# Performance work log

Measured on AMD Instinct MI355X. Metric: run time of the kernel, lower is better.

## Reference

```python
import jax, jax.numpy as jnp
import numpy as np

B, H_IN, H_OUT, SEQ_LEN = 256, 512, 512, 512


def setup_inputs() -> dict:
    key = jax.random.key(0)
    k1, k2, k3, k4, k5 = jax.random.split(key, 5)
    s = 1.0 / np.sqrt(H_OUT)  # torch GRU init scale
    return {
        "x": jax.random.normal(k1, (B, H_IN), dtype=jnp.float32),
        "W_ih": jax.random.uniform(k2, (3 * H_OUT, H_IN), jnp.float32, -s, s),
        "W_hh": jax.random.uniform(k3, (3 * H_OUT, H_OUT), jnp.float32, -s, s),
        "b_ih": jax.random.uniform(k4, (3 * H_OUT,), jnp.float32, -s, s),
        "b_hh": jax.random.uniform(k5, (3 * H_OUT,), jnp.float32, -s, s),
        "seq_len": SEQ_LEN,
    }


def reference(x, W_ih, W_hh, b_ih, b_hh, seq_len):
    # bridge: ReLU, then the same vector is fed at every timestep, so the
    # input-to-hidden projection is computed ONCE and reused across the scan.
    xr = jax.nn.relu(x)                       # [B, H_in]
    gi = xr @ W_ih.T + b_ih                   # [B, 3*H_out], constant over time
    Hh = W_hh.shape[1]
    gi_r, gi_z, gi_n = gi[:, :Hh], gi[:, Hh:2 * Hh], gi[:, 2 * Hh:]

    h0 = jnp.zeros((x.shape[0], Hh), dtype=x.dtype)

    def step(h, _):
        gh = h @ W_hh.T + b_hh                # [B, 3*H_out]
        gh_r, gh_z, gh_n = gh[:, :Hh], gh[:, Hh:2 * Hh], gh[:, 2 * Hh:]
        r = jax.nn.sigmoid(gi_r + gh_r)
        z = jax.nn.sigmoid(gi_z + gh_z)
        n = jnp.tanh(gi_n + r * gh_n)
        h_new = (1.0 - z) * n + z * h
        return h_new, h_new

    _, hs = jax.lax.scan(step, h0, None, length=seq_len)  # [S, B, H_out]
    return jnp.transpose(hs, (1, 0, 2))                   # [B, S, H_out]
```

## Files before the change

kernel.cpp:

```cpp
#include <hip/hip_runtime.h>


typedef __attribute__((ext_vector_type(8))) short short8;
typedef __attribute__((ext_vector_type(4))) float f32x4;
typedef __attribute__((ext_vector_type(4))) unsigned int u32x4;
typedef unsigned short ushort_t;
typedef unsigned int uint_t;
typedef unsigned long long u64_t;

#define NG 16
#define NM 16
#define NB 16
#define NJ 32
#define TPB 384
#define SPIN_MAX (1u << 16)
#define ABORT_IDX 8192
#define GBUF_BASE 16384
#define GRP_U32 4096
#define BUF_U32 65536

#define ALD(P) __hip_atomic_load((P), __ATOMIC_RELAXED, __HIP_MEMORY_SCOPE_AGENT)
#define AST(P, V) __hip_atomic_store((P), (V), __ATOMIC_RELAXED, __HIP_MEMORY_SCOPE_AGENT)

__device__ __forceinline__ ushort_t bf16_rne(float f) {
  uint_t u = __float_as_uint(f);
  return (ushort_t)((u + 0x7fffu + ((u >> 16) & 1u)) >> 16);
}
__device__ __forceinline__ float bf16f(ushort_t h) {
  return __uint_as_float(((uint_t)h) << 16);
}
__device__ __forceinline__ int gRow(int rs, int m) {
  int base = m * NJ;
  if (rs < 32) return base + rs;
  if (rs < 64) return 512 + base + (rs - 32);
  return 1024 + base + (rs - 64);
}

template <bool LO>
__device__ __forceinline__ void loadW(short8* dst, const float* __restrict__ W,
                                      int tile, int m, int lane) {
  int rs = tile * 16 + (lane & 15);
  const float* p = W + (size_t)gRow(rs, m) * 512 + ((lane >> 4) << 3);
#pragma unroll
  for (int c = 0; c < 16; ++c) {
    const float* pc = p + c * 32;
    short8 o;
#pragma unroll
    for (int i = 0; i < 8; ++i) {
      float v = pc[i];
      ushort_t hi = bf16_rne(v);
      o[i] = LO ? (short)bf16_rne(v - bf16f(hi)) : (short)hi;
    }
    dst[c] = o;
  }
}

__global__ __launch_bounds__(TPB, 1) void gru_kernel(
    const float* __restrict__ x, const float* __restrict__ Wih,
    const float* __restrict__ Whh, const float* __restrict__ bih,
    const float* __restrict__ bhh, float* __restrict__ out,
    uint_t* __restrict__ wsp, int NT) {
  __shared__ __align__(16) uint_t s_pb[4096];
  __shared__ __align__(16) uint_t s_xlo[4096];
  __shared__ float s_gi[96 * 17];
  __shared__ float s_gh[96 * 17];
  __shared__ float s_hloc[NB * NJ];
  __shared__ float s_bhh[NJ];
  __shared__ int s_stop;

  const int tid = threadIdx.x;
  const int lane = tid & 63;
  const int w = tid >> 6;
  const int bid = blockIdx.x;
  const int g = bid & 15;
  const int m = bid >> 4;
  const int me = (g << 4) + m;
  if (NT <= 0) return;

  uint_t* flags = wsp;
  uint_t* gbuf = wsp + GBUF_BASE;

  for (int i = tid; i < 1024; i += TPB) {
    int b = i >> 6, k0 = (i & 63) << 3;
    const float* px = x + (size_t)(g * NB + b) * 512 + k0;
    u32x4 vh, vl;
#pragma unroll
    for (int jj = 0; jj < 4; ++jj) {
      float f0 = px[2 * jj], f1 = px[2 * jj + 1];
      f0 = f0 > 0.f ? f0 : 0.f;
      f1 = f1 > 0.f ? f1 : 0.f;
      ushort_t h0 = bf16_rne(f0), h1 = bf16_rne(f1);
      vh[jj] = (uint_t)h0 | ((uint_t)h1 << 16);
      vl[jj] = (uint_t)bf16_rne(f0 - bf16f(h0)) |
               ((uint_t)bf16_rne(f1 - bf16f(h1)) << 16);
    }
    int c = k0 >> 5, kk = k0 & 31;
    int base = c * 1024 + ((((b << 6) + (kk << 1))) ^ ((b & 7) << 4));
    *(u32x4*)((char*)s_pb + base) = vh;
    *(u32x4*)((char*)s_xlo + base) = vl;
  }
  if (tid < NJ) s_bhh[tid] = bhh[1024 + m * NJ + tid];
  if (tid == 0) s_stop = 0;
  __syncthreads();

  short8 wA[16], wB[16];
  const f32x4 vzero = {0.f, 0.f, 0.f, 0.f};
  const int bcol = lane & 15;
  const int roff = ((bcol << 6) + ((lane >> 4) << 4)) ^ ((bcol & 7) << 4);
  const char* pb = (const char*)s_pb;
  const char* pxl = (const char*)s_xlo;

  f32x4 acc0 = vzero, acc1 = vzero;
  if (w < 3) {
    loadW<false>(wA, Wih, 2 * w, m, lane);
    loadW<false>(wB, Wih, 2 * w + 1, m, lane);
    {
      f32x4 a0h = vzero, a0l = vzero, a1h = vzero, a1l = vzero;
#pragma unroll
      for (int c = 0; c < 16; ++c) {
        short8 bh = *(const short8*)(pb + c * 1024 + roff);
        short8 bl = *(const short8*)(pxl + c * 1024 + roff);
        a0h = __builtin_amdgcn_mfma_f32_16x16x32_bf16(wA[c], bh, a0h, 0, 0, 0);
        a1h = __builtin_amdgcn_mfma_f32_16x16x32_bf16(wB[c], bh, a1h, 0, 0, 0);
        a0l = __builtin_amdgcn_mfma_f32_16x16x32_bf16(wA[c], bl, a0l, 0, 0, 0);
        a1l = __builtin_amdgcn_mfma_f32_16x16x32_bf16(wB[c], bl, a1l, 0, 0, 0);
      }
      acc0 = a0h + a0l;
      acc1 = a1h + a1l;
    }
    loadW<true>(wA, Wih, 2 * w, m, lane);
    loadW<true>(wB, Wih, 2 * w + 1, m, lane);
#pragma unroll
    for (int c = 0; c < 16; ++c) {
      short8 bh = *(const short8*)(pb + c * 1024 + roff);
      acc0 = __builtin_amdgcn_mfma_f32_16x16x32_bf16(wA[c], bh, acc0, 0, 0, 0);
      acc1 = __builtin_amdgcn_mfma_f32_16x16x32_bf16(wB[c], bh, acc1, 0, 0, 0);
    }
  }
  __syncthreads();
  if (w < 3) {
    int drow = (lane >> 4) << 2;
#pragma unroll
    for (int q = 0; q < 4; ++q) {
      int rs0 = 2 * w * 16 + drow + q, rs1 = rs0 + 16;
      int g0 = gRow(rs0, m), g1 = gRow(rs1, m);
      s_gi[rs0 * 17 + bcol] = acc0[q] + bih[g0] + (rs0 < 64 ? bhh[g0] : 0.f);
      s_gi[rs1 * 17 + bcol] = acc1[q] + bih[g1] + (rs1 < 64 ? bhh[g1] : 0.f);
    }
    loadW<false>(wA, Whh, 2 * w, m, lane);
    loadW<false>(wB, Whh, 2 * w + 1, m, lane);
  }
  for (int i = tid; i < 4096; i += TPB) s_pb[i] = 0u;
  for (int i = tid; i < NB * NJ; i += TPB) s_hloc[i] = 0.f;
  __syncthreads();

  const size_t outRow = (size_t)NT * 512;
  float* outBase = out + (size_t)(g * NB) * outRow + m * NJ;

  for (int t = 0; t < NT; ++t) {
    if (w < 3) {
      f32x4 aE0 = vzero, aO0 = vzero, aE1 = vzero, aO1 = vzero;
#pragma unroll
      for (int p = 0; p < 16; p += 2) {
        short8 b0 = *(const short8*)(pb + p * 1024 + roff);
        short8 b1 = *(const short8*)(pb + (p + 1) * 1024 + roff);
        aE0 = __builtin_amdgcn_mfma_f32_16x16x32_bf16(wA[p], b0, aE0, 0, 0, 0);
        aE1 = __builtin_amdgcn_mfma_f32_16x16x32_bf16(wB[p], b0, aE1, 0, 0, 0);
        aO0 = __builtin_amdgcn_mfma_f32_16x16x32_bf16(wA[p + 1], b1, aO0, 0, 0, 0);
        aO1 = __builtin_amdgcn_mfma_f32_16x16x32_bf16(wB[p + 1], b1, aO1, 0, 0, 0);
      }
      f32x4 r0 = aE0 + aO0, r1 = aE1 + aO1;
      int drow = (lane >> 4) << 2;
#pragma unroll
      for (int q = 0; q < 4; ++q) {
        s_gh[(2 * w * 16 + drow + q) * 17 + bcol] = r0[q];
        s_gh[((2 * w + 1) * 16 + drow + q) * 17 + bcol] = r1[q];
      }
    }
    __syncthreads();

    const int et = tid - 256;
    float hn[4];
    int eb_ = 0, ej0 = 0;
    if (et >= 0) {
      int b = et >> 3, j0 = (et & 7) << 2;
      eb_ = b;
      ej0 = j0;
#pragma unroll
      for (int e = 0; e < 4; ++e) {
        int j = j0 + e;
        float pr = s_gi[j * 17 + b] + s_gh[j * 17 + b];
        float pz = s_gi[(32 + j) * 17 + b] + s_gh[(32 + j) * 17 + b];
        float r = 1.f / (1.f + __expf(-pr));
        float z = 1.f / (1.f + __expf(-pz));
        float pn =
            s_gi[(64 + j) * 17 + b] + r * (s_gh[(64 + j) * 17 + b] + s_bhh[j]);
        float n = 1.f - 2.f / (1.f + __expf(2.f * pn));
        hn[e] = n + z * (s_hloc[b * 32 + j] - n);
        s_hloc[b * 32 + j] = hn[e];
      }
      uint_t w0 = (uint_t)bf16_rne(hn[0]) | ((uint_t)bf16_rne(hn[1]) << 16);
      uint_t w1 = (uint_t)bf16_rne(hn[2]) | ((uint_t)bf16_rne(hn[3]) << 16);
      u64_t pq = (u64_t)w0 | ((u64_t)w1 << 32);
      u64_t* eb64 =
          (u64_t*)(gbuf + (size_t)((t & 1) ^ 1) * BUF_U32 + g * GRP_U32);
      __hip_atomic_store(eb64 + (m << 7) + (eb_ << 3) + (et & 7), pq,
                         __ATOMIC_RELAXED, __HIP_MEMORY_SCOPE_AGENT);
    }
    __syncthreads();

    if (tid == 256)
      AST(&flags[me << 5], (uint_t)(t + 1));
    if (et >= 0) {
      f32x4 ov = {hn[0], hn[1], hn[2], hn[3]};
      __builtin_nontemporal_store(
          ov,
          (f32x4*)(outBase + (size_t)eb_ * outRow + (size_t)t * 512 + ej0));
    }
    if (w < 4 && t + 1 < NT) {
      const uint_t tgt = (uint_t)(t + 1);
      int ok = 1;
      {
        uint_t sp = 0;
        uint_t* fp = flags + (((g << 4) + (w << 2) + (lane & 3)) << 5);
        for (;;) {
          uint_t v = tgt;
          if (lane < 4) v = ALD(fp);
          if (__all((int)(v >= tgt))) break;
          ++sp;
          uint_t ab = 0;
          if ((sp & 127u) == 0u) {
            ab = ALD(&flags[ABORT_IDX]);
            if (sp > SPIN_MAX) {
              AST(&flags[ABORT_IDX], 1u);
              ab = 1;
            }
          }
          if (__any((int)(ab != 0))) {
            if (lane == 0) s_stop = 1;
            ok = 0;
            break;
          }
          __builtin_amdgcn_s_sleep(1);
        }
      }
      if (ok) {
        const u64_t* srcq =
            (const u64_t*)(gbuf + (size_t)((t + 1) & 1) * BUF_U32 +
                           g * GRP_U32) +
            (w << 9);
#define LDI(k)                                                                 \
  __hip_atomic_load(srcq + lane + ((k) << 6), __ATOMIC_RELAXED,                \
                    __HIP_MEMORY_SCOPE_AGENT)
        u64_t q0 = LDI(0), q1 = LDI(1), q2 = LDI(2), q3 = LDI(3);
        u64_t q4 = LDI(4), q5 = LDI(5), q6 = LDI(6), q7 = LDI(7);
#undef LDI
#define STI(k, qq)                                                             \
  {                                                                            \
    uint_t qb = (uint_t)(((w << 9) + lane + ((k) << 6)) << 3);                 \
    *(u64_t*)((char*)s_pb + (qb ^ (((qb >> 6) & 7u) << 4))) = (qq);            \
  }
        STI(0, q0) STI(1, q1) STI(2, q2) STI(3, q3)
        STI(4, q4) STI(5, q5) STI(6, q6) STI(7, q7)
#undef STI
      }
    }
    __syncthreads();
    if (s_stop) break;
  }
}

extern "C" void kernel_launch(void* const* d_in, const int* in_sizes, int n_in,
                              void* d_out, int out_size, void* d_ws,
                              size_t ws_size, hipStream_t stream) {
  const float* x = (const float*)d_in[0];
  const float* Wih = (const float*)d_in[1];
  const float* Whh = (const float*)d_in[2];
  const float* bih = (const float*)d_in[3];
  const float* bhh = (const float*)d_in[4];
  float* out = (float*)d_out;
  int NT = out_size / (256 * 512);
  uint_t* wsp = (uint_t*)d_ws;
  (void)hipMemsetAsync(d_ws, 0, 65536, stream);
  hipLaunchKernelGGL(gru_kernel, dim3(NG * NM), dim3(TPB), 0, stream, x, Wih,
                     Whh, bih, bhh, out, wsp, NT);
}
```

Before: 1.162 ms.

## Replace post-store barrier and step flag with per-wave checksummed flags

Each epilogue wave now publishes its hidden-state slice together with an XOR checksum in a per-wave, parity-indexed 64-bit flag, right after its data store. This removes the block-wide barrier that sat between the data stores and the flag store. Consumers wait for both wave flags, then reload the data until its checksum matches, which handles the case where the flag becomes visible before the data. This shortens the critical path of each recurrent step. In exchange it adds shuffle reductions, possible reload retries, and a checksum-based correctness argument that could in principle miss a collision.

Result: slower. 1.630 ms (+40.3%).

```diff
diff --git a/kernel.cpp b/kernel.cpp
--- a/kernel.cpp
+++ b/kernel.cpp
@@ -13,7 +13,8 @@
 #define NB 16
 #define NJ 32
 #define TPB 384
-#define SPIN_MAX (1u << 16)
+#define POLL_MAX (1u << 14)
+#define VERIFY_MAX 4096u
 #define ABORT_IDX 8192
 #define GBUF_BASE 16384
 #define GRP_U32 4096
@@ -22,6 +23,9 @@
 #define ALD(P) __hip_atomic_load((P), __ATOMIC_RELAXED, __HIP_MEMORY_SCOPE_AGENT)
 #define AST(P, V) __hip_atomic_store((P), (V), __ATOMIC_RELAXED, __HIP_MEMORY_SCOPE_AGENT)
 
+__device__ __forceinline__ uint_t fold64(u64_t q) {
+  return (uint_t)q ^ (uint_t)(q >> 32);
+}
 __device__ __forceinline__ ushort_t bf16_rne(float f) {
   uint_t u = __float_as_uint(f);
   return (ushort_t)((u + 0x7fffu + ((u >> 16) & 1u)) >> 16);
@@ -77,7 +81,8 @@
   const int me = (g << 4) + m;
   if (NT <= 0) return;
 
-  uint_t* flags = wsp;
+  uint_t* flagsu = wsp;
+  u64_t* flq = (u64_t*)wsp;
   uint_t* gbuf = wsp + GBUF_BASE;
 
   for (int i = tid; i < 1024; i += TPB) {
@@ -158,6 +163,7 @@
   float* outBase = out + (size_t)(g * NB) * outRow + m * NJ;
 
   for (int t = 0; t < NT; ++t) {
+    const int par = (t + 1) & 1;
     if (w < 3) {
       f32x4 aE0 = vzero, aO0 = vzero, aE1 = vzero, aO1 = vzero;
 #pragma unroll
@@ -180,12 +186,9 @@
     __syncthreads();
 
     const int et = tid - 256;
-    float hn[4];
-    int eb_ = 0, ej0 = 0;
     if (et >= 0) {
       int b = et >> 3, j0 = (et & 7) << 2;
-      eb_ = b;
-      ej0 = j0;
+      float hn[4];
 #pragma unroll
       for (int e = 0; e < 4; ++e) {
         int j = j0 + e;
@@ -202,67 +205,106 @@
       uint_t w0 = (uint_t)bf16_rne(hn[0]) | ((uint_t)bf16_rne(hn[1]) << 16);
       uint_t w1 = (uint_t)bf16_rne(hn[2]) | ((uint_t)bf16_rne(hn[3]) << 16);
       u64_t pq = (u64_t)w0 | ((u64_t)w1 << 32);
-      u64_t* eb64 =
-          (u64_t*)(gbuf + (size_t)((t & 1) ^ 1) * BUF_U32 + g * GRP_U32);
-      __hip_atomic_store(eb64 + (m << 7) + (eb_ << 3) + (et & 7), pq,
-                         __ATOMIC_RELAXED, __HIP_MEMORY_SCOPE_AGENT);
-    }
-    __syncthreads();
-
-    if (tid == 256)
-      AST(&flags[me << 5], (uint_t)(t + 1));
-    if (et >= 0) {
+      u64_t* eb64 = (u64_t*)(gbuf + (size_t)par * BUF_U32 + g * GRP_U32);
+      AST(eb64 + (m << 7) + (b << 3) + (et & 7), pq);
+      uint_t c32 = fold64(pq);
+#pragma unroll
+      for (int off = 1; off < 64; off <<= 1) c32 ^= __shfl_xor(c32, off);
+      if (lane == 0) {
+        u64_t f = (u64_t)(uint_t)(t + 1) | ((u64_t)c32 << 32);
+        AST(flq + ((size_t)me << 4) + (par << 1) + (w - 4), f);
+      }
       f32x4 ov = {hn[0], hn[1], hn[2], hn[3]};
       __builtin_nontemporal_store(
-          ov,
-          (f32x4*)(outBase + (size_t)eb_ * outRow + (size_t)t * 512 + ej0));
-    }
+          ov, (f32x4*)(outBase + (size_t)b * outRow + (size_t)t * 512 + j0));
+    }
+
     if (w < 4 && t + 1 < NT) {
       const uint_t tgt = (uint_t)(t + 1);
-      int ok = 1;
+      int aborted = 0;
+      uint_t cs = 0;
       {
+        const u64_t* fq =
+            flq + ((size_t)((g << 4) + (w << 2) + (lane & 3)) << 4) +
+            (par << 1);
         uint_t sp = 0;
-        uint_t* fp = flags + (((g << 4) + (w << 2) + (lane & 3)) << 5);
         for (;;) {
-          uint_t v = tgt;
-          if (lane < 4) v = ALD(fp);
-          if (__all((int)(v >= tgt))) break;
+          int rdy = 1;
+          u64_t f0 = 0, f1 = 0;
+          if (lane < 4) {
+            f0 = ALD(fq);
+            f1 = ALD(fq + 1);
+            rdy = ((uint_t)f0 == tgt) && ((uint_t)f1 == tgt);
+          }
+          if (__all(rdy)) {
+            cs = (uint_t)(f0 >> 32) ^ (uint_t)(f1 >> 32);
+            break;
+          }
           ++sp;
           uint_t ab = 0;
-          if ((sp & 127u) == 0u) {
-            ab = ALD(&flags[ABORT_IDX]);
-            if (sp > SPIN_MAX) {
-              AST(&flags[ABORT_IDX], 1u);
+          if ((sp & 7u) == 0u) {
+            ab = ALD(&flagsu[ABORT_IDX]);
+            if (sp > POLL_MAX) {
+              AST(&flagsu[ABORT_IDX], 1u);
               ab = 1;
             }
           }
           if (__any((int)(ab != 0))) {
             if (lane == 0) s_stop = 1;
-            ok = 0;
+            aborted = 1;
             break;
           }
           __builtin_amdgcn_s_sleep(1);
         }
       }
-      if (ok) {
+      if (!aborted) {
         const u64_t* srcq =
-            (const u64_t*)(gbuf + (size_t)((t + 1) & 1) * BUF_U32 +
-                           g * GRP_U32) +
+            (const u64_t*)(gbuf + (size_t)par * BUF_U32 + g * GRP_U32) +
             (w << 9);
-#define LDI(k)                                                                 \
-  __hip_atomic_load(srcq + lane + ((k) << 6), __ATOMIC_RELAXED,                \
-                    __HIP_MEMORY_SCOPE_AGENT)
-        u64_t q0 = LDI(0), q1 = LDI(1), q2 = LDI(2), q3 = LDI(3);
-        u64_t q4 = LDI(4), q5 = LDI(5), q6 = LDI(6), q7 = LDI(7);
-#undef LDI
+        uint_t att = 0;
+        int good = 0;
+        u64_t q0, q1, q2, q3, q4, q5, q6, q7;
+        for (;;) {
+          q0 = ALD(srcq + lane + 0 * 64);
+          q1 = ALD(srcq + lane + 1 * 64);
+          q2 = ALD(srcq + lane + 2 * 64);
+          q3 = ALD(srcq + lane + 3 * 64);
+          q4 = ALD(srcq + lane + 4 * 64);
+          q5 = ALD(srcq + lane + 5 * 64);
+          q6 = ALD(srcq + lane + 6 * 64);
+          q7 = ALD(srcq + lane + 7 * 64);
+          uint_t c0 = fold64(q0 ^ q1), c1 = fold64(q2 ^ q3);
+          uint_t c2 = fold64(q4 ^ q5), c3 = fold64(q6 ^ q7);
+#pragma unroll
+          for (int off = 1; off < 64; off <<= 1) {
+            c0 ^= __shfl_xor(c0, off);
+            c1 ^= __shfl_xor(c1, off);
+            c2 ^= __shfl_xor(c2, off);
+            c3 ^= __shfl_xor(c3, off);
+          }
+          uint_t mysum =
+              (lane & 2) ? ((lane & 1) ? c3 : c2) : ((lane & 1) ? c1 : c0);
+          int ok = (lane < 4) ? (mysum == cs) : 1;
+          if (__all(ok)) {
+            good = 1;
+            break;
+          }
+          if (++att > VERIFY_MAX) {
+            AST(&flagsu[ABORT_IDX], 1u);
+            if (lane == 0) s_stop = 1;
+            break;
+          }
+        }
+        if (good) {
 #define STI(k, qq)                                                             \
   {                                                                            \
     uint_t qb = (uint_t)(((w << 9) + lane + ((k) << 6)) << 3);                 \
     *(u64_t*)((char*)s_pb + (qb ^ (((qb >> 6) & 7u) << 4))) = (qq);            \
   }
-        STI(0, q0) STI(1, q1) STI(2, q2) STI(3, q3)
-        STI(4, q4) STI(5, q5) STI(6, q6) STI(7, q7)
+          STI(0, q0) STI(1, q1) STI(2, q2) STI(3, q3)
+          STI(4, q4) STI(5, q5) STI(6, q6) STI(7, q7)
 #undef STI
+        }
       }
     }
     __syncthreads();
```

## Replace flag-based inter-block handoff with step-tagged data words polled directly

Applied to the files above, without the earlier changes.

Each hidden-state store now packs 32 bits of bf16 data with a 32-bit timestep tag in a single 64-bit atomic word. Consumers poll the data itself until every tag matches, replacing the separate per-block flag store, the extra __syncthreads before it, and the flag spin followed by a second load. This removes one barrier and one global round trip from each recurrent step. In exchange it doubles the bytes exchanged through the global buffer, makes each poll load 16 words per lane, and adds a fixed sleep before polling starts.

Result: slower. 2.609 ms (+124.5%).

```diff
diff --git a/kernel.cpp b/kernel.cpp
--- a/kernel.cpp
+++ b/kernel.cpp
@@ -13,11 +13,11 @@
 #define NB 16
 #define NJ 32
 #define TPB 384
-#define SPIN_MAX (1u << 16)
+#define SWEEP_MAX 8192u
 #define ABORT_IDX 8192
 #define GBUF_BASE 16384
-#define GRP_U32 4096
-#define BUF_U32 65536
+#define PAR_U64 65536
+#define GRP_U64 4096
 
 #define ALD(P) __hip_atomic_load((P), __ATOMIC_RELAXED, __HIP_MEMORY_SCOPE_AGENT)
 #define AST(P, V) __hip_atomic_store((P), (V), __ATOMIC_RELAXED, __HIP_MEMORY_SCOPE_AGENT)
@@ -74,11 +74,10 @@
   const int bid = blockIdx.x;
   const int g = bid & 15;
   const int m = bid >> 4;
-  const int me = (g << 4) + m;
   if (NT <= 0) return;
 
-  uint_t* flags = wsp;
-  uint_t* gbuf = wsp + GBUF_BASE;
+  uint_t* flagsu = wsp;
+  u64_t* gq = (u64_t*)(wsp + GBUF_BASE);
 
   for (int i = tid; i < 1024; i += TPB) {
     int b = i >> 6, k0 = (i & 63) << 3;
@@ -158,6 +157,7 @@
   float* outBase = out + (size_t)(g * NB) * outRow + m * NJ;
 
   for (int t = 0; t < NT; ++t) {
+    const int par = (t + 1) & 1;
     if (w < 3) {
       f32x4 aE0 = vzero, aO0 = vzero, aE1 = vzero, aO1 = vzero;
 #pragma unroll
@@ -180,12 +180,9 @@
     __syncthreads();
 
     const int et = tid - 256;
-    float hn[4];
-    int eb_ = 0, ej0 = 0;
     if (et >= 0) {
       int b = et >> 3, j0 = (et & 7) << 2;
-      eb_ = b;
-      ej0 = j0;
+      float hn[4];
 #pragma unroll
       for (int e = 0; e < 4; ++e) {
         int j = j0 + e;
@@ -199,70 +196,74 @@
         hn[e] = n + z * (s_hloc[b * 32 + j] - n);
         s_hloc[b * 32 + j] = hn[e];
       }
-      uint_t w0 = (uint_t)bf16_rne(hn[0]) | ((uint_t)bf16_rne(hn[1]) << 16);
-      uint_t w1 = (uint_t)bf16_rne(hn[2]) | ((uint_t)bf16_rne(hn[3]) << 16);
-      u64_t pq = (u64_t)w0 | ((u64_t)w1 << 32);
-      u64_t* eb64 =
-          (u64_t*)(gbuf + (size_t)((t & 1) ^ 1) * BUF_U32 + g * GRP_U32);
-      __hip_atomic_store(eb64 + (m << 7) + (eb_ << 3) + (et & 7), pq,
-                         __ATOMIC_RELAXED, __HIP_MEMORY_SCOPE_AGENT);
-    }
-    __syncthreads();
-
-    if (tid == 256)
-      AST(&flags[me << 5], (uint_t)(t + 1));
-    if (et >= 0) {
+      const u64_t tag = (u64_t)(uint_t)(t + 1) << 32;
+      uint_t d0 = (uint_t)bf16_rne(hn[0]) | ((uint_t)bf16_rne(hn[1]) << 16);
+      uint_t d1 = (uint_t)bf16_rne(hn[2]) | ((uint_t)bf16_rne(hn[3]) << 16);
+      u64_t* dst = gq + (size_t)par * PAR_U64 + g * GRP_U64 + m * 256 +
+                   b * 16 + ((et & 7) << 1);
+      AST(dst, (u64_t)d0 | tag);
+      AST(dst + 1, (u64_t)d1 | tag);
       f32x4 ov = {hn[0], hn[1], hn[2], hn[3]};
       __builtin_nontemporal_store(
-          ov,
-          (f32x4*)(outBase + (size_t)eb_ * outRow + (size_t)t * 512 + ej0));
-    }
+          ov, (f32x4*)(outBase + (size_t)b * outRow + (size_t)t * 512 + j0));
+    }
+
     if (w < 4 && t + 1 < NT) {
       const uint_t tgt = (uint_t)(t + 1);
-      int ok = 1;
-      {
-        uint_t sp = 0;
-        uint_t* fp = flags + (((g << 4) + (w << 2) + (lane & 3)) << 5);
-        for (;;) {
-          uint_t v = tgt;
-          if (lane < 4) v = ALD(fp);
-          if (__all((int)(v >= tgt))) break;
-          ++sp;
-          uint_t ab = 0;
-          if ((sp & 127u) == 0u) {
-            ab = ALD(&flags[ABORT_IDX]);
-            if (sp > SPIN_MAX) {
-              AST(&flags[ABORT_IDX], 1u);
-              ab = 1;
-            }
+      const int p = (w << 2) + (lane >> 4);
+      const int kp = lane & 15;
+      const u64_t* src =
+          gq + (size_t)par * PAR_U64 + g * GRP_U64 + p * 256 + kp;
+      u64_t q0, q1, q2, q3, q4, q5, q6, q7, q8, q9, qA, qB, qC, qD, qE, qF;
+      int good = 0;
+      uint_t sweeps = 0;
+      __builtin_amdgcn_s_sleep(6);
+      for (;;) {
+        q0 = ALD(src + 0 * 16);  q1 = ALD(src + 1 * 16);
+        q2 = ALD(src + 2 * 16);  q3 = ALD(src + 3 * 16);
+        q4 = ALD(src + 4 * 16);  q5 = ALD(src + 5 * 16);
+        q6 = ALD(src + 6 * 16);  q7 = ALD(src + 7 * 16);
+        q8 = ALD(src + 8 * 16);  q9 = ALD(src + 9 * 16);
+        qA = ALD(src + 10 * 16); qB = ALD(src + 11 * 16);
+        qC = ALD(src + 12 * 16); qD = ALD(src + 13 * 16);
+        qE = ALD(src + 14 * 16); qF = ALD(src + 15 * 16);
+        uint_t ok =
+            ((uint_t)(q0 >> 32) == tgt) & ((uint_t)(q1 >> 32) == tgt) &
+            ((uint_t)(q2 >> 32) == tgt) & ((uint_t)(q3 >> 32) == tgt) &
+            ((uint_t)(q4 >> 32) == tgt) & ((uint_t)(q5 >> 32) == tgt) &
+            ((uint_t)(q6 >> 32) == tgt) & ((uint_t)(q7 >> 32) == tgt) &
+            ((uint_t)(q8 >> 32) == tgt) & ((uint_t)(q9 >> 32) == tgt) &
+            ((uint_t)(qA >> 32) == tgt) & ((uint_t)(qB >> 32) == tgt) &
+            ((uint_t)(qC >> 32) == tgt) & ((uint_t)(qD >> 32) == tgt) &
+            ((uint_t)(qE >> 32) == tgt) & ((uint_t)(qF >> 32) == tgt);
+        if (__all((int)ok)) {
+          good = 1;
+          break;
+        }
+        ++sweeps;
+        uint_t ab = 0;
+        if ((sweeps & 7u) == 0u) {
+          ab = ALD(&flagsu[ABORT_IDX]);
+          if (sweeps > SWEEP_MAX) {
+            AST(&flagsu[ABORT_IDX], 1u);
+            ab = 1;
           }
-          if (__any((int)(ab != 0))) {
-            if (lane == 0) s_stop = 1;
-            ok = 0;
-            break;
-          }
-          __builtin_amdgcn_s_sleep(1);
         }
-      }
-      if (ok) {
-        const u64_t* srcq =
-            (const u64_t*)(gbuf + (size_t)((t + 1) & 1) * BUF_U32 +
-                           g * GRP_U32) +
-            (w << 9);
-#define LDI(k)                                                                 \
-  __hip_atomic_load(srcq + lane + ((k) << 6), __ATOMIC_RELAXED,                \
-                    __HIP_MEMORY_SCOPE_AGENT)
-        u64_t q0 = LDI(0), q1 = LDI(1), q2 = LDI(2), q3 = LDI(3);
-        u64_t q4 = LDI(4), q5 = LDI(5), q6 = LDI(6), q7 = LDI(7);
-#undef LDI
-#define STI(k, qq)                                                             \
-  {                                                                            \
-    uint_t qb = (uint_t)(((w << 9) + lane + ((k) << 6)) << 3);                 \
-    *(u64_t*)((char*)s_pb + (qb ^ (((qb >> 6) & 7u) << 4))) = (qq);            \
-  }
-        STI(0, q0) STI(1, q1) STI(2, q2) STI(3, q3)
-        STI(4, q4) STI(5, q5) STI(6, q6) STI(7, q7)
-#undef STI
+        if (__any((int)(ab != 0))) {
+          if (lane == 0) s_stop = 1;
+          break;
+        }
+        __builtin_amdgcn_s_sleep(2);
+      }
+      if (good) {
+#define STW(b, qq)                                                             \
+  *(uint_t*)((char*)s_pb + p * 1024 +                                          \
+             ((((b) << 6) + (kp << 2)) ^ (((b)&7) << 4))) = (uint_t)(qq);
+        STW(0, q0)  STW(1, q1)  STW(2, q2)  STW(3, q3)
+        STW(4, q4)  STW(5, q5)  STW(6, q6)  STW(7, q7)
+        STW(8, q8)  STW(9, q9)  STW(10, qA) STW(11, qB)
+        STW(12, qC) STW(13, qD) STW(14, qE) STW(15, qF)
+#undef STW
       }
     }
     __syncthreads();
```

## Restructure GRU step loop to one barrier with MFMA operands read from global

Applied to the files above, without the earlier changes.

The per-step loop is reordered so the elementwise gate update runs first, on a double-buffered s_gh, and the MMA waves then spin on flags and compute the next step's hidden projection. Each MMA lane loads its bf16 hidden-state operands straight from the global exchange buffer into registers, which removes the LDS staging copy and two of the three __syncthreads per step. Producer waves publish per-wave flags after an explicit vmcnt wait, instead of one flag per block after a barrier. The cost is more global atomic loads per lane, more flag polling, a larger register footprint, and a shorter spin/abort limit.

Result: slower. 2.022 ms (+74.1%).

```diff
diff --git a/kernel.cpp b/kernel.cpp
--- a/kernel.cpp
+++ b/kernel.cpp
@@ -13,14 +13,19 @@
 #define NB 16
 #define NJ 32
 #define TPB 384
-#define SPIN_MAX (1u << 16)
+#define SPIN_MAX (1u << 15)
 #define ABORT_IDX 8192
 #define GBUF_BASE 16384
-#define GRP_U32 4096
-#define BUF_U32 65536
+#define PAR_U64 32768
+#define GRP_U64 2048
 
 #define ALD(P) __hip_atomic_load((P), __ATOMIC_RELAXED, __HIP_MEMORY_SCOPE_AGENT)
 #define AST(P, V) __hip_atomic_store((P), (V), __ATOMIC_RELAXED, __HIP_MEMORY_SCOPE_AGENT)
+#define VMWAIT()                                                               \
+  do {                                                                         \
+    asm volatile("s_waitcnt vmcnt(0)" ::: "memory");                           \
+    __builtin_amdgcn_sched_barrier(0);                                         \
+  } while (0)
 
 __device__ __forceinline__ ushort_t bf16_rne(float f) {
   uint_t u = __float_as_uint(f);
@@ -28,6 +33,15 @@
 }
 __device__ __forceinline__ float bf16f(ushort_t h) {
   return __uint_as_float(((uint_t)h) << 16);
+}
+__device__ __forceinline__ short8 mk8(u64_t a, u64_t b) {
+  union {
+    u64_t q[2];
+    short8 s;
+  } u;
+  u.q[0] = a;
+  u.q[1] = b;
+  return u.s;
 }
 __device__ __forceinline__ int gRow(int rs, int m) {
   int base = m * NJ;
@@ -63,7 +77,7 @@
   __shared__ __align__(16) uint_t s_pb[4096];
   __shared__ __align__(16) uint_t s_xlo[4096];
   __shared__ float s_gi[96 * 17];
-  __shared__ float s_gh[96 * 17];
+  __shared__ float s_gh[2][96 * 17];
   __shared__ float s_hloc[NB * NJ];
   __shared__ float s_bhh[NJ];
   __shared__ int s_stop;
@@ -77,8 +91,8 @@
   const int me = (g << 4) + m;
   if (NT <= 0) return;
 
-  uint_t* flags = wsp;
-  uint_t* gbuf = wsp + GBUF_BASE;
+  uint_t* flagsu = wsp;
+  u64_t* gq = (u64_t*)(wsp + GBUF_BASE);
 
   for (int i = tid; i < 1024; i += TPB) {
     int b = i >> 6, k0 = (i & 63) << 3;
@@ -150,119 +164,105 @@
     loadW<false>(wA, Whh, 2 * w, m, lane);
     loadW<false>(wB, Whh, 2 * w + 1, m, lane);
   }
-  for (int i = tid; i < 4096; i += TPB) s_pb[i] = 0u;
+  for (int i = tid; i < 96 * 17; i += TPB) s_gh[0][i] = 0.f;
   for (int i = tid; i < NB * NJ; i += TPB) s_hloc[i] = 0.f;
   __syncthreads();
 
   const size_t outRow = (size_t)NT * 512;
   float* outBase = out + (size_t)(g * NB) * outRow + m * NJ;
+  const int lofs = ((lane & 15) << 3) + ((lane >> 4) << 1);
 
   for (int t = 0; t < NT; ++t) {
-    if (w < 3) {
-      f32x4 aE0 = vzero, aO0 = vzero, aE1 = vzero, aO1 = vzero;
-#pragma unroll
-      for (int p = 0; p < 16; p += 2) {
-        short8 b0 = *(const short8*)(pb + p * 1024 + roff);
-        short8 b1 = *(const short8*)(pb + (p + 1) * 1024 + roff);
-        aE0 = __builtin_amdgcn_mfma_f32_16x16x32_bf16(wA[p], b0, aE0, 0, 0, 0);
-        aE1 = __builtin_amdgcn_mfma_f32_16x16x32_bf16(wB[p], b0, aE1, 0, 0, 0);
-        aO0 = __builtin_amdgcn_mfma_f32_16x16x32_bf16(wA[p + 1], b1, aO0, 0, 0, 0);
-        aO1 = __builtin_amdgcn_mfma_f32_16x16x32_bf16(wB[p + 1], b1, aO1, 0, 0, 0);
-      }
-      f32x4 r0 = aE0 + aO0, r1 = aE1 + aO1;
-      int drow = (lane >> 4) << 2;
-#pragma unroll
-      for (int q = 0; q < 4; ++q) {
-        s_gh[(2 * w * 16 + drow + q) * 17 + bcol] = r0[q];
-        s_gh[((2 * w + 1) * 16 + drow + q) * 17 + bcol] = r1[q];
-      }
-    }
-    __syncthreads();
-
+    const int xpar = (t + 1) & 1;
     const int et = tid - 256;
-    float hn[4];
-    int eb_ = 0, ej0 = 0;
     if (et >= 0) {
+      const float* ghp = s_gh[t & 1];
       int b = et >> 3, j0 = (et & 7) << 2;
-      eb_ = b;
-      ej0 = j0;
+      float hn[4];
 #pragma unroll
       for (int e = 0; e < 4; ++e) {
         int j = j0 + e;
-        float pr = s_gi[j * 17 + b] + s_gh[j * 17 + b];
-        float pz = s_gi[(32 + j) * 17 + b] + s_gh[(32 + j) * 17 + b];
+        float pr = s_gi[j * 17 + b] + ghp[j * 17 + b];
+        float pz = s_gi[(32 + j) * 17 + b] + ghp[(32 + j) * 17 + b];
         float r = 1.f / (1.f + __expf(-pr));
         float z = 1.f / (1.f + __expf(-pz));
         float pn =
-            s_gi[(64 + j) * 17 + b] + r * (s_gh[(64 + j) * 17 + b] + s_bhh[j]);
+            s_gi[(64 + j) * 17 + b] + r * (ghp[(64 + j) * 17 + b] + s_bhh[j]);
         float n = 1.f - 2.f / (1.f + __expf(2.f * pn));
         hn[e] = n + z * (s_hloc[b * 32 + j] - n);
         s_hloc[b * 32 + j] = hn[e];
       }
-      uint_t w0 = (uint_t)bf16_rne(hn[0]) | ((uint_t)bf16_rne(hn[1]) << 16);
-      uint_t w1 = (uint_t)bf16_rne(hn[2]) | ((uint_t)bf16_rne(hn[3]) << 16);
-      u64_t pq = (u64_t)w0 | ((u64_t)w1 << 32);
-      u64_t* eb64 =
-          (u64_t*)(gbuf + (size_t)((t & 1) ^ 1) * BUF_U32 + g * GRP_U32);
-      __hip_atomic_store(eb64 + (m << 7) + (eb_ << 3) + (et & 7), pq,
-                         __ATOMIC_RELAXED, __HIP_MEMORY_SCOPE_AGENT);
-    }
-    __syncthreads();
-
-    if (tid == 256)
-      AST(&flags[me << 5], (uint_t)(t + 1));
-    if (et >= 0) {
+      if (t + 1 < NT) {
+        uint_t d0 = (uint_t)bf16_rne(hn[0]) | ((uint_t)bf16_rne(hn[1]) << 16);
+        uint_t d1 = (uint_t)bf16_rne(hn[2]) | ((uint_t)bf16_rne(hn[3]) << 16);
+        u64_t pq = (u64_t)d0 | ((u64_t)d1 << 32);
+        u64_t* dst = gq + (size_t)xpar * PAR_U64 + g * GRP_U64 + (m << 7) +
+                     (b << 3) + (et & 7);
+        AST(dst, pq);
+        VMWAIT();
+        if (lane == 0)
+          AST(&flagsu[(me << 5) + ((w - 4) << 3)], (uint_t)(t + 1));
+      }
       f32x4 ov = {hn[0], hn[1], hn[2], hn[3]};
       __builtin_nontemporal_store(
-          ov,
-          (f32x4*)(outBase + (size_t)eb_ * outRow + (size_t)t * 512 + ej0));
-    }
-    if (w < 4 && t + 1 < NT) {
+          ov, (f32x4*)(outBase + (size_t)b * outRow + (size_t)t * 512 + j0));
+    }
+
+    if (w < 3 && t + 1 < NT) {
       const uint_t tgt = (uint_t)(t + 1);
-      int ok = 1;
+      int aborted = 0;
       {
         uint_t sp = 0;
-        uint_t* fp = flags + (((g << 4) + (w << 2) + (lane & 3)) << 5);
+        uint_t* fp =
+            flagsu + ((((g << 4) + (lane >> 1)) << 5) + ((lane & 1) << 3));
         for (;;) {
           uint_t v = tgt;
-          if (lane < 4) v = ALD(fp);
+          if (lane < 32) v = ALD(fp);
           if (__all((int)(v >= tgt))) break;
           ++sp;
           uint_t ab = 0;
-          if ((sp & 127u) == 0u) {
-            ab = ALD(&flags[ABORT_IDX]);
+          if ((sp & 15u) == 0u) {
+            ab = ALD(&flagsu[ABORT_IDX]);
             if (sp > SPIN_MAX) {
-              AST(&flags[ABORT_IDX], 1u);
+              AST(&flagsu[ABORT_IDX], 1u);
               ab = 1;
             }
           }
           if (__any((int)(ab != 0))) {
             if (lane == 0) s_stop = 1;
-            ok = 0;
+            aborted = 1;
             break;
           }
           __builtin_amdgcn_s_sleep(1);
         }
       }
-      if (ok) {
-        const u64_t* srcq =
-            (const u64_t*)(gbuf + (size_t)((t + 1) & 1) * BUF_U32 +
-                           g * GRP_U32) +
-            (w << 9);
-#define LDI(k)                                                                 \
-  __hip_atomic_load(srcq + lane + ((k) << 6), __ATOMIC_RELAXED,                \
-                    __HIP_MEMORY_SCOPE_AGENT)
-        u64_t q0 = LDI(0), q1 = LDI(1), q2 = LDI(2), q3 = LDI(3);
-        u64_t q4 = LDI(4), q5 = LDI(5), q6 = LDI(6), q7 = LDI(7);
-#undef LDI
-#define STI(k, qq)                                                             \
-  {                                                                            \
-    uint_t qb = (uint_t)(((w << 9) + lane + ((k) << 6)) << 3);                 \
-    *(u64_t*)((char*)s_pb + (qb ^ (((qb >> 6) & 7u) << 4))) = (qq);            \
-  }
-        STI(0, q0) STI(1, q1) STI(2, q2) STI(3, q3)
-        STI(4, q4) STI(5, q5) STI(6, q6) STI(7, q7)
-#undef STI
+      if (!aborted) {
+        const u64_t* src =
+            gq + (size_t)xpar * PAR_U64 + g * GRP_U64 + lofs;
+        u64_t qv[32];
+#pragma unroll
+        for (int p = 0; p < 16; ++p) {
+          qv[2 * p] = ALD(src + (p << 7));
+          qv[2 * p + 1] = ALD(src + (p << 7) + 1);
+        }
+        f32x4 aE0 = vzero, aO0 = vzero, aE1 = vzero, aO1 = vzero;
+#pragma unroll
+        for (int p = 0; p < 16; p += 2) {
+          short8 b0 = mk8(qv[2 * p], qv[2 * p + 1]);
+          short8 b1 = mk8(qv[2 * p + 2], qv[2 * p + 3]);
+          aE0 = __builtin_amdgcn_mfma_f32_16x16x32_bf16(wA[p], b0, aE0, 0, 0, 0);
+          aE1 = __builtin_amdgcn_mfma_f32_16x16x32_bf16(wB[p], b0, aE1, 0, 0, 0);
+          aO0 = __builtin_amdgcn_mfma_f32_16x16x32_bf16(wA[p + 1], b1, aO0, 0, 0, 0);
+          aO1 = __builtin_amdgcn_mfma_f32_16x16x32_bf16(wB[p + 1], b1, aO1, 0, 0, 0);
+        }
+        f32x4 r0 = aE0 + aO0, r1 = aE1 + aO1;
+        float* ghn = s_gh[xpar];
+        int drow = (lane >> 4) << 2;
+#pragma unroll
+        for (int q = 0; q < 4; ++q) {
+          ghn[(2 * w * 16 + drow + q) * 17 + bcol] = r0[q];
+          ghn[((2 * w + 1) * 16 + drow + q) * 17 + bcol] = r1[q];
+        }
       }
     }
     __syncthreads();
```
